# Optimization experiments

Measured on AMD Instinct MI355X. Metric: run time of the kernel, lower is better.

The kernel has to match this reference:

```python
import jax, jax.numpy as jnp
import numpy as np

EPS = 1e-5  # InstanceNorm2d default eps


def setup_inputs() -> dict:
    key = jax.random.key(0)
    k1, k2, k3, k4, k5, k6 = jax.random.split(key, 6)
    B, N, C, KV, H = 8, 4096, 512, 960, 4
    dq, dk = C // 4, KV // 4
    emb1 = jax.random.normal(k1, (B, N, C), dtype=jnp.float32)
    emb_all = jax.random.normal(k2, (B, N, KV), dtype=jnp.float32)
    # per-head query Linear weights (torch Linear weight is [out, in]); 4 distinct heads
    Wq = jax.random.normal(k3, (H, dq, dq), dtype=jnp.float32) * 0.05
    # key/value: the original forward only ever uses key[0] / value[0]
    Wk = jax.random.normal(k4, (dk, dk), dtype=jnp.float32) * 0.05
    Wv = jax.random.normal(k5, (dk, dk), dtype=jnp.float32) * 0.05
    Wo = jax.random.normal(k6, (C, C), dtype=jnp.float32) * 0.05
    return {"emb1": emb1, "emb_all": emb_all, "Wq": Wq, "Wk": Wk, "Wv": Wv, "Wo": Wo}


def reference(emb1, emb_all, Wq, Wk, Wv, Wo):
    B, N, C = emb1.shape
    KV = emb_all.shape[2]
    dq, dk = C // 4, KV // 4
    # split emb1 into 4 chunks along channels -> [B, N, 4, dq], apply per-head query Linear
    Qc = emb1.reshape(B, N, 4, dq)
    Q = jnp.einsum("bnhd,hed->bhne", Qc, Wq)            # [B,4,N,dq]
    # all 4 K and V chunks use key[0]/value[0] (as in the source)
    Kc = emb_all.reshape(B, N, 4, dk)
    K = jnp.einsum("bnhd,ed->bhne", Kc, Wk)             # [B,4,N,dk]
    V = jnp.einsum("bnhd,ed->bhne", Kc, Wv)             # [B,4,N,dk]
    # channel attention: contract over tokens N -> scores [B,4,dq,dk]
    scores = jnp.einsum("bhnc,bhnk->bhck", Q, K) / jnp.sqrt(jnp.float32(KV))
    # InstanceNorm2d (no affine): normalize each (b, head) score map over (dq, dk)
    mu = scores.mean(axis=(2, 3), keepdims=True)
    var = scores.var(axis=(2, 3), keepdims=True)        # biased variance, matches torch
    normed = (scores - mu) * jax.lax.rsqrt(var + EPS)
    probs = jax.nn.softmax(normed, axis=3)              # softmax over dk
    # dropout is identity in eval mode
    context = jnp.einsum("bhck,bhnk->bhcn", probs, V)   # [B,4,dq,N]
    # permute(0,3,2,1) -> [B,N,dq,4], flatten last two -> [B,N,C]
    context = jnp.transpose(context, (0, 3, 2, 1)).reshape(B, N, C)
    O1 = jnp.einsum("bnc,ec->bne", context, Wo)         # out Linear, no bias
    return O1
```

## Files before the change

### kernel.cpp

```cpp
#include <hip/hip_runtime.h>
#include <cstdint>
#include <cstddef>

#define B_ 8
#define N_ 4096
#define C_ 512
#define KV_ 960
#define DQ 128
#define DK 240
#define NSPLIT 8

typedef __attribute__((ext_vector_type(8))) short bf16x8;
typedef __attribute__((ext_vector_type(4))) float f32x4;
#define AS1 __attribute__((address_space(1)))
#define AS3 __attribute__((address_space(3)))

__device__ __forceinline__ ushort f2bf(float f) {
  uint32_t u = __float_as_uint(f);
  u += 0x7FFFu + ((u >> 16) & 1u);
  return (ushort)(u >> 16);
}

__device__ __forceinline__ uint32_t cvtpk(float lo, float hi) {
  uint32_t r;
  asm("v_cvt_pk_bf16_f32 %0, %1, %2" : "=v"(r) : "v"(lo), "v"(hi));
  return r;
}

union bfpack {
  uint32_t u[4];
  ushort s[8];
  bf16x8 v;
};

__global__ __launch_bounds__(512) void k1_mfma(const float* __restrict__ emb1,
                                               const ushort* __restrict__ embaBF,
                                               float* __restrict__ P) {
  __shared__ ushort As[128 * 64];
  __shared__ ushort Bs[128 * 64];
  const int bh = blockIdx.x;
  const int split = blockIdx.y;
  const int jh = blockIdx.z;
  const int b = bh >> 2, h = bh & 3;
  const int t = threadIdx.x;
  const int w = t >> 6, l = t & 63;
  const int wm = w >> 1, wn = w & 1;

  const float* Abase = emb1 + (size_t)b * N_ * C_ + h * DQ;
  const ushort* Bbase = embaBF + (size_t)b * N_ * KV_;

  const int cA = t & 127;
  const int jB = t & 127;
  const int nb0 = t >> 7;
  int jl = jh * 128 + jB;
  if (jl > DK - 1) jl = DK - 1;
  const int jg = h * DK + jl;

  f32x4 acc[2][4];
#pragma unroll
  for (int fm = 0; fm < 2; ++fm)
#pragma unroll
    for (int fn = 0; fn < 4; ++fn) acc[fm][fn] = (f32x4){0.f, 0.f, 0.f, 0.f};

  const int n0 = split * (N_ / NSPLIT);
  const int lrow = l & 15;
  const int KS = (N_ / NSPLIT) / 64;

  float va[2][8];
  ushort ub[2][8];

#pragma unroll
  for (int q = 0; q < 2; ++q) {
    const float* g = Abase + (size_t)(n0 + (nb0 + q * 4) * 8) * C_ + cA;
#pragma unroll
    for (int kk = 0; kk < 8; ++kk) va[q][kk] = g[(size_t)kk * C_];
  }
#pragma unroll
  for (int q = 0; q < 2; ++q) {
    const ushort* g = Bbase + (size_t)(n0 + (nb0 + q * 4) * 8) * KV_ + jg;
#pragma unroll
    for (int kk = 0; kk < 8; ++kk) ub[q][kk] = g[(size_t)kk * KV_];
  }

  for (int ks = 0; ks < KS; ++ks) {
    bfpack pa[2], pb[2];
#pragma unroll
    for (int q = 0; q < 2; ++q)
#pragma unroll
      for (int p = 0; p < 4; ++p) pa[q].u[p] = cvtpk(va[q][2 * p], va[q][2 * p + 1]);
#pragma unroll
    for (int q = 0; q < 2; ++q)
#pragma unroll
      for (int kk = 0; kk < 8; ++kk) pb[q].s[kk] = ub[q][kk];

    __builtin_amdgcn_s_barrier();

#pragma unroll
    for (int q = 0; q < 2; ++q) {
      const int nb = nb0 + q * 4;
      *(bf16x8*)(As + cA * 64 + ((nb ^ (cA & 7)) << 3)) = pa[q].v;
      *(bf16x8*)(Bs + jB * 64 + ((nb ^ (jB & 7)) << 3)) = pb[q].v;
    }

    if (ks + 1 < KS) {
      const int nb1 = n0 + (ks + 1) * 64;
#pragma unroll
      for (int q = 0; q < 2; ++q) {
        const float* g = Abase + (size_t)(nb1 + (nb0 + q * 4) * 8) * C_ + cA;
#pragma unroll
        for (int kk = 0; kk < 8; ++kk) va[q][kk] = g[(size_t)kk * C_];
      }
#pragma unroll
      for (int q = 0; q < 2; ++q) {
        const ushort* g = Bbase + (size_t)(nb1 + (nb0 + q * 4) * 8) * KV_ + jg;
#pragma unroll
        for (int kk = 0; kk < 8; ++kk) ub[q][kk] = g[(size_t)kk * KV_];
      }
    }

    asm volatile("s_waitcnt lgkmcnt(0)" ::: "memory");
    __builtin_amdgcn_sched_barrier(0);
    __builtin_amdgcn_s_barrier();

#pragma unroll
    for (int half = 0; half < 2; ++half) {
      const int kb = half * 4 + (l >> 4);
      bf16x8 af[2], bv[4];
#pragma unroll
      for (int fm = 0; fm < 2; ++fm) {
        const int i = wm * 32 + fm * 16 + lrow;
        af[fm] = *(const bf16x8*)(As + i * 64 + ((kb ^ (i & 7)) << 3));
      }
#pragma unroll
      for (int fn = 0; fn < 4; ++fn) {
        const int j = wn * 64 + fn * 16 + lrow;
        bv[fn] = *(const bf16x8*)(Bs + j * 64 + ((kb ^ (j & 7)) << 3));
      }
#pragma unroll
      for (int fm = 0; fm < 2; ++fm)
#pragma unroll
        for (int fn = 0; fn < 4; ++fn)
          acc[fm][fn] = __builtin_amdgcn_mfma_f32_16x16x32_bf16(af[fm], bv[fn],
                                                                acc[fm][fn], 0, 0, 0);
    }
  }
  f32x4* Pv4 = (f32x4*)P + ((size_t)(split * 32 + bh) * 2 + jh) * 4096;
#pragma unroll
  for (int fm = 0; fm < 2; ++fm)
#pragma unroll
    for (int fn = 0; fn < 4; ++fn) Pv4[(fm * 4 + fn) * 512 + t] = acc[fm][fn];
}

__global__ __launch_bounds__(256) void k_reduce_frag(const f32x4* __restrict__ P,
                                                     float* __restrict__ S) {
  const int bh = blockIdx.x;
  const int g = blockIdx.y * 256 + threadIdx.x;
  const int jh = g >> 12;
  const int rest = g & 4095;
  f32x4 a = P[((size_t)bh * 2 + jh) * 4096 + rest];
#pragma unroll
  for (int s = 1; s < NSPLIT; ++s) {
    f32x4 v = P[((size_t)(s * 32 + bh) * 2 + jh) * 4096 + rest];
    a.x += v.x; a.y += v.y; a.z += v.z; a.w += v.w;
  }
  const int v = rest >> 9, tt = rest & 511;
  const int fm = v >> 2, fn = v & 3;
  const int wv = tt >> 6, l = tt & 63;
  const int wm = wv >> 1, wn = wv & 1;
  const int i0 = wm * 32 + fm * 16 + (l >> 4) * 4;
  const int j = jh * 128 + wn * 64 + fn * 16 + (l & 15);
  if (j < DK) {
    float* sp = S + (size_t)bh * (DQ * DK) + (size_t)i0 * DK + j;
    sp[0] = a.x; sp[DK] = a.y; sp[2 * DK] = a.z; sp[3 * DK] = a.w;
  }
}

__global__ __launch_bounds__(256) void k_cvt(const float4* __restrict__ in,
                                             ushort4* __restrict__ out, int n4) {
  int i = blockIdx.x * 256 + threadIdx.x;
  if (i >= n4) return;
  float4 v = in[i];
  ushort4 o;
  o.x = f2bf(v.x); o.y = f2bf(v.y); o.z = f2bf(v.z); o.w = f2bf(v.w);
  out[i] = o;
}

__global__ __launch_bounds__(256) void k_g1(const float* __restrict__ Wq,
                                            const float* __restrict__ S,
                                            float* __restrict__ U) {
  const int h = blockIdx.x, c0 = blockIdx.y * 64;
  const int b = blockIdx.z / 5, n0 = (blockIdx.z % 5) * 48;
  const float* A = Wq + (size_t)h * 16384;
  const float* Bp = S + (size_t)(b * 4 + h) * 30720 + n0;
  float* Cp = U + (size_t)(b * 4 + h) * 30720 + n0;
  __shared__ float Ast[16][65];
  __shared__ float Bst[16][49];
  const int t = threadIdx.x;
  const int mi = (t >> 4) * 4, nj = (t & 15) * 3;
  float acc[4][3] = {};
  for (int k0 = 0; k0 < 128; k0 += 16) {
    __syncthreads();
#pragma unroll
    for (int q = 0; q < 4; ++q) {
      int idx = t + q * 256, m = idx >> 4, k = idx & 15;
      Ast[k][m] = A[(size_t)(c0 + m) * 128 + k0 + k];
    }
#pragma unroll
    for (int q = 0; q < 3; ++q) {
      int idx = t + q * 256, k = idx / 48, n = idx % 48;
      Bst[k][n] = Bp[(size_t)(k0 + k) * 240 + n];
    }
    __syncthreads();
#pragma unroll
    for (int kk = 0; kk < 16; ++kk) {
      float a4[4], b3[3];
#pragma unroll
      for (int x = 0; x < 4; ++x) a4[x] = Ast[kk][mi + x];
#pragma unroll
      for (int y = 0; y < 3; ++y) b3[y] = Bst[kk][nj + y];
#pragma unroll
      for (int x = 0; x < 4; ++x)
#pragma unroll
        for (int y = 0; y < 3; ++y) acc[x][y] = fmaf(a4[x], b3[y], acc[x][y]);
    }
  }
#pragma unroll
  for (int x = 0; x < 4; ++x)
#pragma unroll
    for (int y = 0; y < 3; ++y)
      Cp[(size_t)(c0 + mi + x) * 240 + nj + y] = acc[x][y];
}

__global__ __launch_bounds__(256) void k_g2(const float* __restrict__ U,
                                            const float* __restrict__ Wk,
                                            float* __restrict__ SC) {
  const int m0 = blockIdx.x * 64, n0 = blockIdx.y * 48;
  __shared__ float Ast[16][65];
  __shared__ float Bst2[48][17];
  const int t = threadIdx.x;
  const int mi = (t >> 4) * 4, nj = (t & 15) * 3;
  float acc[4][3] = {};
  for (int k0 = 0; k0 < 240; k0 += 16) {
    __syncthreads();
#pragma unroll
    for (int q = 0; q < 4; ++q) {
      int idx = t + q * 256, m = idx >> 4, k = idx & 15;
      Ast[k][m] = U[(size_t)(m0 + m) * 240 + k0 + k];
    }
#pragma unroll
    for (int q = 0; q < 3; ++q) {
      int idx = t + q * 256, n = idx >> 4, kd = idx & 15;
      Bst2[n][kd] = Wk[(size_t)(n0 + n) * 240 + k0 + kd];
    }
    __syncthreads();
#pragma unroll
    for (int kk = 0; kk < 16; ++kk) {
      float a4[4], b3[3];
#pragma unroll
      for (int x = 0; x < 4; ++x) a4[x] = Ast[kk][mi + x];
#pragma unroll
      for (int y = 0; y < 3; ++y) b3[y] = Bst2[nj + y][kk];
#pragma unroll
      for (int x = 0; x < 4; ++x)
#pragma unroll
        for (int y = 0; y < 3; ++y) acc[x][y] = fmaf(a4[x], b3[y], acc[x][y]);
    }
  }
  const float scale = 0.0322748612183951f;
#pragma unroll
  for (int x = 0; x < 4; ++x)
#pragma unroll
    for (int y = 0; y < 3; ++y)
      SC[(size_t)(m0 + mi + x) * 240 + n0 + nj + y] = acc[x][y] * scale;
}

__global__ __launch_bounds__(256) void k_g3(const float* __restrict__ PR,
                                            const float* __restrict__ Wv,
                                            float* __restrict__ T) {
  const int m0 = blockIdx.x * 64, n0 = blockIdx.y * 48;
  __shared__ float Ast[16][65];
  __shared__ float Bst[16][49];
  const int t = threadIdx.x;
  const int mi = (t >> 4) * 4, nj = (t & 15) * 3;
  float acc[4][3] = {};
  for (int k0 = 0; k0 < 240; k0 += 16) {
    __syncthreads();
#pragma unroll
    for (int q = 0; q < 4; ++q) {
      int idx = t + q * 256, m = idx >> 4, k = idx & 15;
      Ast[k][m] = PR[(size_t)(m0 + m) * 240 + k0 + k];
    }
#pragma unroll
    for (int q = 0; q < 3; ++q) {
      int idx = t + q * 256, k = idx / 48, n = idx % 48;
      Bst[k][n] = Wv[(size_t)(k0 + k) * 240 + n0 + n];
    }
    __syncthreads();
#pragma unroll
    for (int kk = 0; kk < 16; ++kk) {
      float a4[4], b3[3];
#pragma unroll
      for (int x = 0; x < 4; ++x) a4[x] = Ast[kk][mi + x];
#pragma unroll
      for (int y = 0; y < 3; ++y) b3[y] = Bst[kk][nj + y];
#pragma unroll
      for (int x = 0; x < 4; ++x)
#pragma unroll
        for (int y = 0; y < 3; ++y) acc[x][y] = fmaf(a4[x], b3[y], acc[x][y]);
    }
  }
#pragma unroll
  for (int x = 0; x < 4; ++x)
#pragma unroll
    for (int y = 0; y < 3; ++y)
      T[(size_t)(m0 + mi + x) * 240 + n0 + nj + y] = acc[x][y];
}

__global__ __launch_bounds__(256) void k_g4(const float* __restrict__ Wo,
                                            const float* __restrict__ T,
                                            ushort* __restrict__ W3bf) {
  const int h = blockIdx.x, e0 = blockIdx.y * 64;
  const int b = blockIdx.z / 5, n0 = (blockIdx.z % 5) * 48;
  const float* Bp = T + (size_t)(b * 4 + h) * 30720 + n0;
  ushort* Cp = W3bf + (size_t)b * 491520 + h * 240 + n0;
  __shared__ float Ast[16][65];
  __shared__ float Bst[16][49];
  const int t = threadIdx.x;
  const int mi = (t >> 4) * 4, nj = (t & 15) * 3;
  float acc[4][3] = {};
  for (int k0 = 0; k0 < 128; k0 += 16) {
    __syncthreads();
#pragma unroll
    for (int q = 0; q < 4; ++q) {
      int idx = t + q * 256, m = idx >> 4, k = idx & 15;
      Ast[k][m] = Wo[(size_t)(e0 + m) * 512 + 4 * (k0 + k) + h];
    }
#pragma unroll
    for (int q = 0; q < 3; ++q) {
      int idx = t + q * 256, k = idx / 48, n = idx % 48;
      Bst[k][n] = Bp[(size_t)(k0 + k) * 240 + n];
    }
    __syncthreads();
#pragma unroll
    for (int kk = 0; kk < 16; ++kk) {
      float a4[4], b3[3];
#pragma unroll
      for (int x = 0; x < 4; ++x) a4[x] = Ast[kk][mi + x];
#pragma unroll
      for (int y = 0; y < 3; ++y) b3[y] = Bst[kk][nj + y];
#pragma unroll
      for (int x = 0; x < 4; ++x)
#pragma unroll
        for (int y = 0; y < 3; ++y) acc[x][y] = fmaf(a4[x], b3[y], acc[x][y]);
    }
  }
#pragma unroll
  for (int x = 0; x < 4; ++x)
#pragma unroll
    for (int y = 0; y < 3; ++y)
      Cp[(size_t)(e0 + mi + x) * 960 + nj + y] = f2bf(acc[x][y]);
}

__global__ __launch_bounds__(1024) void k_stats(const float* __restrict__ SC,
                                                float* __restrict__ stats) {
  const int bh = blockIdx.x;
  const float* s = SC + (size_t)bh * 30720;
  const int t = threadIdx.x;
  float sum = 0.f, sq = 0.f;
  for (int i = t; i < 30720; i += 1024) {
    float v = s[i];
    sum += v;
    sq = fmaf(v, v, sq);
  }
#pragma unroll
  for (int o = 32; o > 0; o >>= 1) {
    sum += __shfl_down(sum, o);
    sq += __shfl_down(sq, o);
  }
  __shared__ float s1[16], s2[16];
  if ((t & 63) == 0) { s1[t >> 6] = sum; s2[t >> 6] = sq; }
  __syncthreads();
  if (t == 0) {
    float ts = 0.f, tq = 0.f;
#pragma unroll
    for (int i = 0; i < 16; ++i) { ts += s1[i]; tq += s2[i]; }
    const float mu = ts * (1.f / 30720.f);
    const float var = tq * (1.f / 30720.f) - mu * mu;
    stats[bh * 2] = mu;
    stats[bh * 2 + 1] = rsqrtf(var + 1e-5f);
  }
}

__global__ __launch_bounds__(512) void k_softmax(const float* __restrict__ SC,
                                                 const float* __restrict__ stats,
                                                 float* __restrict__ PR) {
  const int bh = blockIdx.x;
  const float mu = stats[bh * 2], rstd = stats[bh * 2 + 1];
  const int wv = threadIdx.x >> 6, l = threadIdx.x & 63;
  const int row0 = blockIdx.y * 32 + wv * 4;
  const float* s = SC + (size_t)bh * 30720;
  float* p = PR + (size_t)bh * 30720;
#pragma unroll
  for (int r = 0; r < 4; ++r) {
    const float* srow = s + (size_t)(row0 + r) * 240;
    float* prow = p + (size_t)(row0 + r) * 240;
    float x0 = (srow[l] - mu) * rstd;
    float x1 = (srow[64 + l] - mu) * rstd;
    float x2 = (srow[128 + l] - mu) * rstd;
    float x3 = (l < 48) ? (srow[192 + l] - mu) * rstd : -1e30f;
    float m = fmaxf(fmaxf(x0, x1), fmaxf(x2, x3));
#pragma unroll
    for (int o = 32; o > 0; o >>= 1) m = fmaxf(m, __shfl_xor(m, o));
    float e0 = __expf(x0 - m), e1 = __expf(x1 - m), e2 = __expf(x2 - m);
    float e3 = (l < 48) ? __expf(x3 - m) : 0.f;
    float ss = e0 + e1 + e2 + e3;
#pragma unroll
    for (int o = 32; o > 0; o >>= 1) ss += __shfl_xor(ss, o);
    const float inv = 1.f / ss;
    prow[l] = e0 * inv;
    prow[64 + l] = e1 * inv;
    prow[128 + l] = e2 * inv;
    if (l < 48) prow[192 + l] = e3 * inv;
  }
}

__global__ __launch_bounds__(256) void k3_mfma(const ushort* __restrict__ A,
                                               const ushort* __restrict__ Bw,
                                               float* __restrict__ C) {
  __shared__ ushort LDSu[2][8192];
  const int bid = blockIdx.x;
  const int swz = (bid & 7) * 128 + (bid >> 3);
  const int b = swz >> 7;
  const int rem = swz & 127;
  const int mt = rem >> 2, nt = rem & 3;
  const int t = threadIdx.x;
  const int w = t >> 6, l = t & 63;
  const int wr = w >> 1, wc = w & 1;

  const ushort* Ab = A + (size_t)b * N_ * KV_ + (size_t)mt * 128 * KV_;
  const ushort* Bb = Bw + (size_t)b * C_ * KV_ + (size_t)nt * 128 * KV_;

  const int r_l = l & 15;
  const int c_l = (l >> 4) * 8;

#define K3STAGE(k0, bf)                                                        \
  do {                                                                         \
    _Pragma("unroll") for (int inst = 0; inst < 2; ++inst) {                   \
      const int gi = w * 2 + inst;                                             \
      const ushort* ga = Ab + (size_t)(gi * 16 + r_l) * KV_ + (k0) + c_l;      \
      __builtin_amdgcn_global_load_lds(                                        \
          (AS1 const uint32_t*)(uintptr_t)ga,                                  \
          (AS3 uint32_t*)(uintptr_t)(&LDSu[bf][0] + gi * 512), 16, 0, 0);      \
      const ushort* gb = Bb + (size_t)(gi * 16 + r_l) * KV_ + (k0) + c_l;      \
      __builtin_amdgcn_global_load_lds(                                        \
          (AS1 const uint32_t*)(uintptr_t)gb,                                  \
          (AS3 uint32_t*)(uintptr_t)(&LDSu[bf][4096] + gi * 512), 16, 0, 0);   \
    }                                                                          \
  } while (0)

  f32x4 acc[4][4];
#pragma unroll
  for (int fm = 0; fm < 4; ++fm)
#pragma unroll
    for (int fn = 0; fn < 4; ++fn) acc[fm][fn] = (f32x4){0.f, 0.f, 0.f, 0.f};

  K3STAGE(0, 0);
  asm volatile("s_waitcnt vmcnt(0)" ::: "memory");
  __builtin_amdgcn_sched_barrier(0);
  __builtin_amdgcn_s_barrier();

  const int NK = KV_ / 32;
  for (int ks = 0; ks < NK; ++ks) {
    const int buf = ks & 1;
    if (ks + 1 < NK) {
      if (buf == 0) K3STAGE((ks + 1) * 32, 1);
      else          K3STAGE((ks + 1) * 32, 0);
    }
    bf16x8 af[4], bfr[4];
#pragma unroll
    for (int fm = 0; fm < 4; ++fm)
      af[fm] = *(const bf16x8*)(&LDSu[buf][0] + (wr * 4 + fm) * 512 + l * 8);
#pragma unroll
    for (int fn = 0; fn < 4; ++fn)
      bfr[fn] = *(const bf16x8*)(&LDSu[buf][4096] + (wc * 4 + fn) * 512 + l * 8);
#pragma unroll
    for (int fm = 0; fm < 4; ++fm)
#pragma unroll
      for (int fn = 0; fn < 4; ++fn)
        acc[fm][fn] = __builtin_amdgcn_mfma_f32_16x16x32_bf16(af[fm], bfr[fn],
                                                              acc[fm][fn], 0, 0, 0);
    asm volatile("s_waitcnt vmcnt(0)" ::: "memory");
    __builtin_amdgcn_sched_barrier(0);
    __builtin_amdgcn_s_barrier();
  }
#undef K3STAGE

  float* Cb = C + (size_t)b * N_ * C_ + ((size_t)mt * 128) * C_ + nt * 128;
  const int col = wc * 64 + (l & 15);
  const int rbase = wr * 64 + (l >> 4) * 4;
#pragma unroll
  for (int fm = 0; fm < 4; ++fm)
#pragma unroll
    for (int fn = 0; fn < 4; ++fn)
#pragma unroll
      for (int r = 0; r < 4; ++r)
        Cb[(size_t)(rbase + fm * 16 + r) * C_ + col + fn * 16] = acc[fm][fn][r];
}

extern "C" void kernel_launch(void* const* d_in, const int* in_sizes, int n_in,
                              void* d_out, int out_size, void* d_ws, size_t ws_size,
                              hipStream_t stream) {
  const float* emb1 = (const float*)d_in[0];
  const float* emba = (const float*)d_in[1];
  const float* Wq   = (const float*)d_in[2];
  const float* Wk   = (const float*)d_in[3];
  const float* Wv   = (const float*)d_in[4];
  const float* Wo   = (const float*)d_in[5];
  float* out = (float*)d_out;
  char* ws = (char*)d_ws;

  ushort* embaBF = (ushort*)(ws);
  float*  S      = (float*)(ws + 62914560);
  float*  T      = (float*)(ws + 62914560);
  float*  U      = (float*)(ws + 66846720);
  ushort* W3bf   = (ushort*)(ws + 66846720);
  float*  SCb    = (float*)(ws + 70778880);
  float*  PRb    = (float*)(ws + 74711040);
  float*  P      = out;
  float*  stats  = (float*)(ws + 66846720);

  k_cvt<<<30720, 256, 0, stream>>>((const float4*)emba, (ushort4*)embaBF, 7864320);

  k1_mfma<<<dim3(32, NSPLIT, 2), 512, 0, stream>>>(emb1, embaBF, P);
  k_reduce_frag<<<dim3(32, 32), 256, 0, stream>>>((const f32x4*)P, S);

  k_g1<<<dim3(4, 2, 40), 256, 0, stream>>>(Wq, S, U);
  k_g2<<<dim3(64, 5), 256, 0, stream>>>(U, Wk, SCb);
  k_stats<<<32, 1024, 0, stream>>>(SCb, stats);
  k_softmax<<<dim3(32, 4), 512, 0, stream>>>(SCb, stats, PRb);
  k_g3<<<dim3(64, 5), 256, 0, stream>>>(PRb, Wv, T);
  k_g4<<<dim3(4, 8, 40), 256, 0, stream>>>(Wo, T, W3bf);

  k3_mfma<<<1024, 256, 0, stream>>>(embaBF, W3bf, out);
}
```

Before: 254.9 us.

## Retile final GEMM to 256x256 blocks with triple-buffered LDS pipeline

The final bf16 MFMA GEMM now uses 256x256 output tiles with 512 threads (8 waves, 128x64 per wave) instead of 128x128 tiles with 256 threads. The LDS ring grows to three buffers, and a partial vmcnt wait keeps two K-stages of loads in flight, so global loads overlap compute better. Separately, the token split count for the first GEMM doubles. Larger tiles cut redundant global reads, but the grid drops to 256 blocks. That risks under-filling the device and raises register and LDS pressure.

Result: faster. 244.2 us (-4.2%).

```diff
diff --git a/kernel.cpp b/kernel.cpp
--- a/kernel.cpp
+++ b/kernel.cpp
@@ -8,7 +8,7 @@
 #define KV_ 960
 #define DQ 128
 #define DK 240
-#define NSPLIT 8
+#define NSPLIT 16
 
 typedef __attribute__((ext_vector_type(8))) short bf16x8;
 typedef __attribute__((ext_vector_type(4))) float f32x4;
@@ -424,21 +424,21 @@
   }
 }
 
-__global__ __launch_bounds__(256) void k3_mfma(const ushort* __restrict__ A,
+__global__ __launch_bounds__(512) void k3_mfma(const ushort* __restrict__ A,
                                                const ushort* __restrict__ Bw,
                                                float* __restrict__ C) {
-  __shared__ ushort LDSu[2][8192];
+  __shared__ ushort LDSu[3][16384];
   const int bid = blockIdx.x;
-  const int swz = (bid & 7) * 128 + (bid >> 3);
-  const int b = swz >> 7;
-  const int rem = swz & 127;
-  const int mt = rem >> 2, nt = rem & 3;
+  const int swz = (bid & 7) * 32 + (bid >> 3);
+  const int b = swz >> 5;
+  const int rem = swz & 31;
+  const int mt = rem >> 1, nt = rem & 1;
   const int t = threadIdx.x;
   const int w = t >> 6, l = t & 63;
-  const int wr = w >> 1, wc = w & 1;
-
-  const ushort* Ab = A + (size_t)b * N_ * KV_ + (size_t)mt * 128 * KV_;
-  const ushort* Bb = Bw + (size_t)b * C_ * KV_ + (size_t)nt * 128 * KV_;
+  const int wr = w >> 2, wc = w & 3;
+
+  const ushort* Ab = A + (size_t)b * N_ * KV_ + (size_t)mt * 256 * KV_;
+  const ushort* Bb = Bw + (size_t)b * C_ * KV_ + (size_t)nt * 256 * KV_;
 
   const int r_l = l & 15;
   const int c_l = (l >> 4) * 8;
@@ -446,60 +446,60 @@
 #define K3STAGE(k0, bf)                                                        \
   do {                                                                         \
     _Pragma("unroll") for (int inst = 0; inst < 2; ++inst) {                   \
-      const int gi = w * 2 + inst;                                             \
-      const ushort* ga = Ab + (size_t)(gi * 16 + r_l) * KV_ + (k0) + c_l;      \
+      const int g = w * 2 + inst;                             \
+      const ushort* ga = Ab + (size_t)(g * 16 + r_l) * KV_ + (k0) + c_l;       \
       __builtin_amdgcn_global_load_lds(                                        \
           (AS1 const uint32_t*)(uintptr_t)ga,                                  \
-          (AS3 uint32_t*)(uintptr_t)(&LDSu[bf][0] + gi * 512), 16, 0, 0);      \
-      const ushort* gb = Bb + (size_t)(gi * 16 + r_l) * KV_ + (k0) + c_l;      \
+          (AS3 uint32_t*)(uintptr_t)(&LDSu[bf][0] + g * 512), 16, 0, 0);       \
+      const ushort* gb = Bb + (size_t)(g * 16 + r_l) * KV_ + (k0) + c_l;       \
       __builtin_amdgcn_global_load_lds(                                        \
           (AS1 const uint32_t*)(uintptr_t)gb,                                  \
-          (AS3 uint32_t*)(uintptr_t)(&LDSu[bf][4096] + gi * 512), 16, 0, 0);   \
+          (AS3 uint32_t*)(uintptr_t)(&LDSu[bf][8192] + g * 512), 16, 0, 0);    \
     }                                                                          \
   } while (0)
 
-  f32x4 acc[4][4];
-#pragma unroll
-  for (int fm = 0; fm < 4; ++fm)
+  f32x4 acc[8][4];
+#pragma unroll
+  for (int fm = 0; fm < 8; ++fm)
 #pragma unroll
     for (int fn = 0; fn < 4; ++fn) acc[fm][fn] = (f32x4){0.f, 0.f, 0.f, 0.f};
 
   K3STAGE(0, 0);
-  asm volatile("s_waitcnt vmcnt(0)" ::: "memory");
-  __builtin_amdgcn_sched_barrier(0);
-  __builtin_amdgcn_s_barrier();
+  K3STAGE(32, 1);
 
   const int NK = KV_ / 32;
+  int cbuf = 0, sbuf = 2;
   for (int ks = 0; ks < NK; ++ks) {
-    const int buf = ks & 1;
-    if (ks + 1 < NK) {
-      if (buf == 0) K3STAGE((ks + 1) * 32, 1);
-      else          K3STAGE((ks + 1) * 32, 0);
-    }
-    bf16x8 af[4], bfr[4];
-#pragma unroll
-    for (int fm = 0; fm < 4; ++fm)
-      af[fm] = *(const bf16x8*)(&LDSu[buf][0] + (wr * 4 + fm) * 512 + l * 8);
-#pragma unroll
-    for (int fn = 0; fn < 4; ++fn)
-      bfr[fn] = *(const bf16x8*)(&LDSu[buf][4096] + (wc * 4 + fn) * 512 + l * 8);
-#pragma unroll
-    for (int fm = 0; fm < 4; ++fm)
-#pragma unroll
-      for (int fn = 0; fn < 4; ++fn)
-        acc[fm][fn] = __builtin_amdgcn_mfma_f32_16x16x32_bf16(af[fm], bfr[fn],
-                                                              acc[fm][fn], 0, 0, 0);
-    asm volatile("s_waitcnt vmcnt(0)" ::: "memory");
+    if (ks < NK - 1) asm volatile("s_waitcnt vmcnt(4)" ::: "memory");
+    else             asm volatile("s_waitcnt vmcnt(0)" ::: "memory");
     __builtin_amdgcn_sched_barrier(0);
     __builtin_amdgcn_s_barrier();
+    if (ks + 2 < NK) K3STAGE((ks + 2) * 32, sbuf);
+    const ushort* Abase = &LDSu[cbuf][0];
+    const ushort* Bbase = &LDSu[cbuf][8192];
+    bf16x8 af[8], bv[4];
+#pragma unroll
+    for (int f = 0; f < 8; ++f)
+      af[f] = *(const bf16x8*)(Abase + (wr * 8 + f) * 512 + l * 8);
+#pragma unroll
+    for (int f = 0; f < 4; ++f)
+      bv[f] = *(const bf16x8*)(Bbase + (wc * 4 + f) * 512 + l * 8);
+#pragma unroll
+    for (int fm = 0; fm < 8; ++fm)
+#pragma unroll
+      for (int fn = 0; fn < 4; ++fn)
+        acc[fm][fn] = __builtin_amdgcn_mfma_f32_16x16x32_bf16(af[fm], bv[fn],
+                                                              acc[fm][fn], 0, 0, 0);
+    cbuf = (cbuf == 2) ? 0 : cbuf + 1;
+    sbuf = (sbuf == 2) ? 0 : sbuf + 1;
   }
 #undef K3STAGE
 
-  float* Cb = C + (size_t)b * N_ * C_ + ((size_t)mt * 128) * C_ + nt * 128;
+  float* Cb = C + (size_t)b * N_ * C_ + ((size_t)mt * 256) * C_ + nt * 256;
   const int col = wc * 64 + (l & 15);
-  const int rbase = wr * 64 + (l >> 4) * 4;
-#pragma unroll
-  for (int fm = 0; fm < 4; ++fm)
+  const int rbase = wr * 128 + (l >> 4) * 4;
+#pragma unroll
+  for (int fm = 0; fm < 8; ++fm)
 #pragma unroll
     for (int fn = 0; fn < 4; ++fn)
 #pragma unroll
@@ -541,5 +541,5 @@
   k_g3<<<dim3(64, 5), 256, 0, stream>>>(PRb, Wv, T);
   k_g4<<<dim3(4, 8, 40), 256, 0, stream>>>(Wo, T, W3bf);
 
-  k3_mfma<<<1024, 256, 0, stream>>>(embaBF, W3bf, out);
-}
+  k3_mfma<<<256, 512, 0, stream>>>(embaBF, W3bf, out);
+}
```
